# Kernel tuning notes

Hardware: AMD Instinct MI355X
Metric: run time of the kernel (lower is better)

Reference implementation:

```python
import jax, jax.numpy as jnp
import numpy as np

B, IN, OUT, BR = 64, 8192, 2048, 4
VTH = 0.5
_SQRT_2PI = float(np.sqrt(2.0 * np.pi))


def _gauss(x, mu, sigma):
    return jnp.exp(-((x - mu) ** 2) / (2.0 * sigma ** 2)) / _SQRT_2PI / sigma


@jax.custom_vjp
def act_fun(x):
    return (x > 0.0).astype(x.dtype)


def _act_fwd(x):
    return act_fun(x), x


def _act_bwd(x, g):
    lens, scale, hight, gamma = 0.5, 6.0, 0.15, 0.5
    temp = (_gauss(x, 0.0, lens) * (1.0 + hight)
            - _gauss(x, lens, scale * lens) * hight
            - _gauss(x, -lens, scale * lens) * hight)
    return (g * temp * gamma,)


act_fun.defvjp(_act_fwd, _act_bwd)


def setup_inputs() -> dict:
    key = jax.random.key(0)
    ks = jax.random.split(key, 8)
    fan_in = IN
    bound = 1.0 / np.sqrt(fan_in)
    return {
        "input_spike": jax.random.uniform(ks[0], (B, IN), dtype=jnp.float32),
        "mem": jax.random.uniform(ks[1], (B, OUT), dtype=jnp.float32),
        "spike": jax.random.uniform(ks[2], (B, OUT), dtype=jnp.float32),
        "d_input": jnp.zeros((B, OUT, BR), dtype=jnp.float32),
        "v_th": jnp.ones((B, OUT), dtype=jnp.float32) * VTH,
        "W": jax.random.uniform(ks[3], (OUT * BR, IN), minval=-bound, maxval=bound, dtype=jnp.float32),
        "b": jax.random.uniform(ks[4], (OUT * BR,), minval=-bound, maxval=bound, dtype=jnp.float32),
        "tau_m": jax.random.uniform(ks[5], (OUT,), minval=0.0, maxval=4.0, dtype=jnp.float32),
        "tau_n": jax.random.uniform(ks[6], (OUT, BR), minval=0.0, maxval=4.0, dtype=jnp.float32),
    }


def reference(input_spike, mem, spike, d_input, v_th, W, b, tau_m, tau_n):
    R_m = 1.0
    batch = input_spike.shape[0]
    out_dim, branch = tau_n.shape
    in_dim = W.shape[1]  # padded input size
    chunk = in_dim // branch
    # pad input to in_dim (pad == 0 for these dims, kept for generality)
    pad = in_dim - input_spike.shape[1]
    k = jnp.pad(input_spike.astype(jnp.float32), ((0, 0), (0, pad)))
    # block-masked linear: mask keeps, for neuron o / branch j, only column block j.
    # Equivalent to taking the diagonal blocks of W reshaped [out, branch, branch, chunk].
    W_diag = jnp.einsum("obbc->obc", W.reshape(out_dim, branch, branch, chunk))
    y = jnp.einsum("obc,nbc->nob", W_diag, k.reshape(batch, branch, chunk))
    y = y + b.reshape(out_dim, branch)  # [B, out, branch]
    # per-branch dendritic decay
    beta = jax.nn.sigmoid(tau_n)
    d_new = beta * d_input + (1.0 - beta) * y
    l_input = d_new.sum(axis=2)  # [B, out]
    # LIF with soft reset
    alpha = jax.nn.sigmoid(tau_m)
    mem_new = mem * alpha + (1.0 - alpha) * R_m * l_input - v_th * spike
    spike_new = act_fun(mem_new - v_th)
    return mem_new, spike_new
```

## Files before the change

### kernel.cpp

```cpp
#include <hip/hip_runtime.h>
#include <math.h>

#define BATCH   64
#define IN_DIM  8192
#define OUT_DIM 2048
#define BRANCH  4
#define CHUNK   2048
#define NSEG    2
#define KSEG    1024
#define KT      128
#define NT      8

typedef __attribute__((ext_vector_type(8))) short short8;
typedef __attribute__((ext_vector_type(4))) short short4v;
typedef __attribute__((ext_vector_type(4))) float f32x4;

__device__ __forceinline__ float sigmoidf_(float x) {
    return 1.0f / (1.0f + expf(-x));
}

__device__ __forceinline__ unsigned rne_bf16(float f) {
    unsigned u = __float_as_uint(f);
    return (u + 0x7fffu + ((u >> 16) & 1u)) >> 16;
}

#define LBAR()                                                   \
    do {                                                         \
        asm volatile("s_waitcnt lgkmcnt(0)" ::: "memory");       \
        __builtin_amdgcn_s_barrier();                            \
        asm volatile("" ::: "memory");                           \
    } while (0)

__global__ __launch_bounds__(256) void prep_x(const float* __restrict__ X,
                                              short8* __restrict__ Xfh,
                                              short8* __restrict__ Xfl) {
    const int gid = blockIdx.x * 256 + threadIdx.x;
    const int l  = gid & 63;
    const int kk = (gid >> 6) & 63;
    const int s  = (gid >> 12) & 3;
    const int j  = gid >> 14;
    const int n  = s * 16 + (l & 15);
    const int k0 = kk * 32 + ((l >> 4) << 3);
    const float* p = X + (size_t)n * IN_DIM + j * CHUNK + k0;
    const f32x4 a = *(const f32x4*)p;
    const f32x4 c = *(const f32x4*)(p + 4);
    float v[8] = {a[0], a[1], a[2], a[3], c[0], c[1], c[2], c[3]};
    short8 h, lo;
#pragma unroll
    for (int e = 0; e < 8; ++e) {
        unsigned hb = rne_bf16(v[e]);
        float fh = __uint_as_float(hb << 16);
        unsigned lb = rne_bf16(v[e] - fh);
        h[e]  = (short)hb;
        lo[e] = (short)lb;
    }
    Xfh[gid] = h;
    Xfl[gid] = lo;
}

__device__ __forceinline__ void stage_store(char* Wh, char* Wl, const f32x4* wr,
                                            int wbyte0, int swz, int kq) {
#pragma unroll
    for (int i = 0; i < 4; ++i) {
        unsigned hb[4], lb[4];
#pragma unroll
        for (int e = 0; e < 4; ++e) {
            const float f  = wr[i][e];
            const unsigned u  = __float_as_uint(f);
            const float fl = f - __uint_as_float(u & 0xffff0000u);
            hb[e] = u >> 16;
            lb[e] = __float_as_uint(fl) >> 16;
        }
        short4v vh = { (short)hb[0], (short)hb[1], (short)hb[2], (short)hb[3] };
        short4v vl = { (short)lb[0], (short)lb[1], (short)lb[2], (short)lb[3] };
        const int kb   = (kq << 5) + (i << 3);
        const int byte = wbyte0 + (kb ^ swz);
        *(short4v*)(Wh + byte) = vh;
        *(short4v*)(Wl + byte) = vl;
    }
}

__global__ __launch_bounds__(256) void dend_gemm(const short8* __restrict__ Xfh,
                                                 const short8* __restrict__ Xfl,
                                                 const float*  __restrict__ W,
                                                 float* __restrict__ Yp) {
    __shared__ __align__(16) char WhL[2][32 * 256];
    __shared__ __align__(16) char WlL[2][32 * 256];

    const int t    = threadIdx.x;
    const int bid  = blockIdx.x;
    const int j    = bid & 3;
    const int o0   = ((bid >> 2) & 63) << 5;
    const int ks   = bid >> 8;
    const int lane = t & 63;
    const int wv   = t >> 6;

    const int ri  = t >> 3;
    const int kq  = t & 7;
    const float* wsrc = W + (size_t)((o0 + ri) * 4 + j) * IN_DIM
                          + j * CHUNK + ks * KSEG + kq * 16;
    const int wbyte0 = ri << 8;
    const int swz    = (ri & 15) << 4;

    const short8* pAh = Xfh + (j * 4 + wv) * 4096 + ks * 2048 + lane;
    const short8* pAl = Xfl + (j * 4 + wv) * 4096 + ks * 2048 + lane;

    const int o_l   = lane & 15;
    const int bswz  = o_l << 4;
    const int kgrp  = (lane >> 4) << 4;
    const int b0row = o_l << 8;
    const int b1row = (o_l + 16) << 8;

    f32x4 acc0 = {0.f, 0.f, 0.f, 0.f};
    f32x4 acc1 = {0.f, 0.f, 0.f, 0.f};

    f32x4  wr[4];
    short8 Ah0[4], Al0[4], Ah1[4], Al1[4];

#pragma unroll
    for (int i = 0; i < 4; ++i)
        wr[i] = *(const f32x4*)(wsrc + i * 4);
    stage_store(WhL[0], WlL[0], wr, wbyte0, swz, kq);
#pragma unroll
    for (int i = 0; i < 4; ++i)
        wr[i] = *(const f32x4*)(wsrc + KT + i * 4);
#pragma unroll
    for (int i = 0; i < 4; ++i) { Ah0[i] = pAh[i * 64];       Al0[i] = pAl[i * 64]; }
#pragma unroll
    for (int i = 0; i < 4; ++i) { Ah1[i] = pAh[(4 + i) * 64]; Al1[i] = pAl[(4 + i) * 64]; }
    LBAR();

#define BODY(kt, AH, AL)                                                            \
  {                                                                                 \
    if ((kt) + 1 < NT)                                                              \
        stage_store(WhL[((kt) + 1) & 1], WlL[((kt) + 1) & 1], wr, wbyte0, swz, kq); \
    if ((kt) + 2 < NT) {                                                            \
        _Pragma("unroll")                                                           \
        for (int i = 0; i < 4; ++i)                                                 \
            wr[i] = *(const f32x4*)(wsrc + ((kt) + 2) * KT + i * 4);                \
    }                                                                               \
    _Pragma("unroll")                                                               \
    for (int st = 0; st < 4; ++st) {                                                \
        const int off = ((st << 6) + kgrp) ^ bswz;                                  \
        short8 bh0 = *(const short8*)(&WhL[(kt) & 1][b0row + off]);                 \
        short8 bl0 = *(const short8*)(&WlL[(kt) & 1][b0row + off]);                 \
        short8 bh1 = *(const short8*)(&WhL[(kt) & 1][b1row + off]);                 \
        short8 bl1 = *(const short8*)(&WlL[(kt) & 1][b1row + off]);                 \
        acc0 = __builtin_amdgcn_mfma_f32_16x16x32_bf16(AH[st], bh0, acc0, 0, 0, 0); \
        acc1 = __builtin_amdgcn_mfma_f32_16x16x32_bf16(AH[st], bh1, acc1, 0, 0, 0); \
        acc0 = __builtin_amdgcn_mfma_f32_16x16x32_bf16(AL[st], bh0, acc0, 0, 0, 0); \
        acc1 = __builtin_amdgcn_mfma_f32_16x16x32_bf16(AL[st], bh1, acc1, 0, 0, 0); \
        acc0 = __builtin_amdgcn_mfma_f32_16x16x32_bf16(AH[st], bl0, acc0, 0, 0, 0); \
        acc1 = __builtin_amdgcn_mfma_f32_16x16x32_bf16(AH[st], bl1, acc1, 0, 0, 0); \
    }                                                                               \
    if ((kt) + 2 < NT) {                                                            \
        _Pragma("unroll")                                                           \
        for (int i = 0; i < 4; ++i) {                                               \
            AH[i] = pAh[(((kt) + 2) * 4 + i) * 64];                                 \
            AL[i] = pAl[(((kt) + 2) * 4 + i) * 64];                                 \
        }                                                                           \
    }                                                                               \
    LBAR();                                                                         \
  }

#pragma unroll 1
    for (int kt = 0; kt < NT; kt += 2) {
        BODY(kt,     Ah0, Al0)
        BODY(kt + 1, Ah1, Al1)
    }
#undef BODY

    float (*Ys)[65] = (float (*)[65])(&WhL[0][0]);
    {
        const int rb = (wv << 4) + ((lane >> 4) << 2);
#pragma unroll
        for (int r = 0; r < 4; ++r) {
            Ys[o_l][rb + r]      = acc0[r];
            Ys[o_l + 16][rb + r] = acc1[r];
        }
    }
    __syncthreads();
#pragma unroll
    for (int p = 0; p < 8; ++p) {
        const int e  = t + (p << 8);
        const int oo = e & 31;
        const int n  = e >> 5;
        Yp[(size_t)(((ks * BATCH + n) << 2) + j) * OUT_DIM + o0 + oo] = Ys[oo][n];
    }
}

__global__ __launch_bounds__(256) void lif_pointwise(
    const float* __restrict__ Yp,
    const float* __restrict__ mem,
    const float* __restrict__ spike,
    const float* __restrict__ d_input,
    const float* __restrict__ v_th,
    const float* __restrict__ b,
    const float* __restrict__ tau_m,
    const float* __restrict__ tau_n,
    float* __restrict__ out)
{
    const int idx = blockIdx.x * 256 + threadIdx.x;
    const int o   = idx & (OUT_DIM - 1);
    const int n   = idx >> 11;

    const float4 tn = ((const float4*)tau_n)[o];
    const float4 bb = ((const float4*)b)[o];
    const float4 di = ((const float4*)d_input)[idx];

    float y0 = 0.f, y1 = 0.f, y2 = 0.f, y3 = 0.f;
#pragma unroll
    for (int s = 0; s < NSEG; ++s) {
        const size_t base = (size_t)((s * BATCH + n) << 2) * OUT_DIM + o;
        y0 += Yp[base];
        y1 += Yp[base + OUT_DIM];
        y2 += Yp[base + 2 * OUT_DIM];
        y3 += Yp[base + 3 * OUT_DIM];
    }

    float l = 0.0f;
    { const float bt = sigmoidf_(tn.x); l += bt * di.x + (1.0f - bt) * (y0 + bb.x); }
    { const float bt = sigmoidf_(tn.y); l += bt * di.y + (1.0f - bt) * (y1 + bb.y); }
    { const float bt = sigmoidf_(tn.z); l += bt * di.z + (1.0f - bt) * (y2 + bb.z); }
    { const float bt = sigmoidf_(tn.w); l += bt * di.w + (1.0f - bt) * (y3 + bb.w); }

    const float alpha = sigmoidf_(tau_m[o]);
    const float vt    = v_th[idx];
    const float m     = mem[idx] * alpha + (1.0f - alpha) * l - vt * spike[idx];

    out[idx] = m;
    out[BATCH * OUT_DIM + idx] = (m - vt) > 0.0f ? 1.0f : 0.0f;
}

extern "C" void kernel_launch(void* const* d_in, const int* in_sizes, int n_in,
                              void* d_out, int out_size, void* d_ws, size_t ws_size,
                              hipStream_t stream) {
    const float* X     = (const float*)d_in[0];
    const float* mem   = (const float*)d_in[1];
    const float* spike = (const float*)d_in[2];
    const float* dinp  = (const float*)d_in[3];
    const float* vth   = (const float*)d_in[4];
    const float* W     = (const float*)d_in[5];
    const float* b     = (const float*)d_in[6];
    const float* tm    = (const float*)d_in[7];
    const float* tn    = (const float*)d_in[8];
    float* out = (float*)d_out;

    short8* Xfh = (short8*)d_ws;
    short8* Xfl = (short8*)((char*)d_ws + (1u << 20));
    float*  Yp  = (float*)((char*)d_ws + (2u << 20));

    prep_x<<<256, 256, 0, stream>>>(X, Xfh, Xfl);
    dend_gemm<<<512, 256, 0, stream>>>(Xfh, Xfl, W, Yp);
    lif_pointwise<<<512, 256, 0, stream>>>(Yp, mem, spike, dinp, vth, b, tm, tn, out);
}
```

Baseline: 27.51 us.

## Double K tile to 256 and interleave A-fragment prefetch within each tile

Doubles the K-tile depth staged through LDS from 128 to 256, halving the number of barrier-separated iterations, and doubles the per-thread W register staging. The A-fragment loads are restructured so the second half of each tile is fetched while the first half computes, and the next tile's first half is fetched during the second half. This aims to cut barrier and sync overhead and improve overlap of global loads with MFMA. In exchange it doubles LDS use to 64KB and raises register pressure, which may reduce occupancy. The swizzle still only XORs the low 16-byte bits within the wider 512-byte rows.

```diff
diff --git a/kernel.cpp b/kernel.cpp
--- a/kernel.cpp
+++ b/kernel.cpp
@@ -8,8 +8,8 @@
 #define CHUNK   2048
 #define NSEG    2
 #define KSEG    1024
-#define KT      128
-#define NT      8
+#define KT      256
+#define NT      4
 
 typedef __attribute__((ext_vector_type(8))) short short8;
 typedef __attribute__((ext_vector_type(4))) short short4v;
@@ -61,7 +61,7 @@
 __device__ __forceinline__ void stage_store(char* Wh, char* Wl, const f32x4* wr,
                                             int wbyte0, int swz, int kq) {
 #pragma unroll
-    for (int i = 0; i < 4; ++i) {
+    for (int i = 0; i < 8; ++i) {
         unsigned hb[4], lb[4];
 #pragma unroll
         for (int e = 0; e < 4; ++e) {
@@ -73,7 +73,7 @@
         }
         short4v vh = { (short)hb[0], (short)hb[1], (short)hb[2], (short)hb[3] };
         short4v vl = { (short)lb[0], (short)lb[1], (short)lb[2], (short)lb[3] };
-        const int kb   = (kq << 5) + (i << 3);
+        const int kb   = (kq << 6) + (i << 3);
         const int byte = wbyte0 + (kb ^ swz);
         *(short4v*)(Wh + byte) = vh;
         *(short4v*)(Wl + byte) = vl;
@@ -84,8 +84,8 @@
                                                  const short8* __restrict__ Xfl,
                                                  const float*  __restrict__ W,
                                                  float* __restrict__ Yp) {
-    __shared__ __align__(16) char WhL[2][32 * 256];
-    __shared__ __align__(16) char WlL[2][32 * 256];
+    __shared__ __align__(16) char WhL[2][32 * 512];
+    __shared__ __align__(16) char WlL[2][32 * 512];
 
     const int t    = threadIdx.x;
     const int bid  = blockIdx.x;
@@ -98,8 +98,8 @@
     const int ri  = t >> 3;
     const int kq  = t & 7;
     const float* wsrc = W + (size_t)((o0 + ri) * 4 + j) * IN_DIM
-                          + j * CHUNK + ks * KSEG + kq * 16;
-    const int wbyte0 = ri << 8;
+                          + j * CHUNK + ks * KSEG + kq * 32;
+    const int wbyte0 = ri << 9;
     const int swz    = (ri & 15) << 4;
 
     const short8* pAh = Xfh + (j * 4 + wv) * 4096 + ks * 2048 + lane;
@@ -108,67 +108,71 @@
     const int o_l   = lane & 15;
     const int bswz  = o_l << 4;
     const int kgrp  = (lane >> 4) << 4;
-    const int b0row = o_l << 8;
-    const int b1row = (o_l + 16) << 8;
+    const int b0row = o_l << 9;
+    const int b1row = (o_l + 16) << 9;
 
     f32x4 acc0 = {0.f, 0.f, 0.f, 0.f};
     f32x4 acc1 = {0.f, 0.f, 0.f, 0.f};
 
-    f32x4  wr[4];
+    f32x4  wr[8];
     short8 Ah0[4], Al0[4], Ah1[4], Al1[4];
 
 #pragma unroll
-    for (int i = 0; i < 4; ++i)
+    for (int i = 0; i < 8; ++i)
         wr[i] = *(const f32x4*)(wsrc + i * 4);
     stage_store(WhL[0], WlL[0], wr, wbyte0, swz, kq);
 #pragma unroll
-    for (int i = 0; i < 4; ++i)
+    for (int i = 0; i < 8; ++i)
         wr[i] = *(const f32x4*)(wsrc + KT + i * 4);
 #pragma unroll
-    for (int i = 0; i < 4; ++i) { Ah0[i] = pAh[i * 64];       Al0[i] = pAl[i * 64]; }
-#pragma unroll
-    for (int i = 0; i < 4; ++i) { Ah1[i] = pAh[(4 + i) * 64]; Al1[i] = pAl[(4 + i) * 64]; }
+    for (int i = 0; i < 4; ++i) { Ah0[i] = pAh[i * 64]; Al0[i] = pAl[i * 64]; }
     LBAR();
 
-#define BODY(kt, AH, AL)                                                            \
-  {                                                                                 \
-    if ((kt) + 1 < NT)                                                              \
-        stage_store(WhL[((kt) + 1) & 1], WlL[((kt) + 1) & 1], wr, wbyte0, swz, kq); \
-    if ((kt) + 2 < NT) {                                                            \
-        _Pragma("unroll")                                                           \
-        for (int i = 0; i < 4; ++i)                                                 \
-            wr[i] = *(const f32x4*)(wsrc + ((kt) + 2) * KT + i * 4);                \
-    }                                                                               \
-    _Pragma("unroll")                                                               \
-    for (int st = 0; st < 4; ++st) {                                                \
-        const int off = ((st << 6) + kgrp) ^ bswz;                                  \
-        short8 bh0 = *(const short8*)(&WhL[(kt) & 1][b0row + off]);                 \
-        short8 bl0 = *(const short8*)(&WlL[(kt) & 1][b0row + off]);                 \
-        short8 bh1 = *(const short8*)(&WhL[(kt) & 1][b1row + off]);                 \
-        short8 bl1 = *(const short8*)(&WlL[(kt) & 1][b1row + off]);                 \
-        acc0 = __builtin_amdgcn_mfma_f32_16x16x32_bf16(AH[st], bh0, acc0, 0, 0, 0); \
-        acc1 = __builtin_amdgcn_mfma_f32_16x16x32_bf16(AH[st], bh1, acc1, 0, 0, 0); \
-        acc0 = __builtin_amdgcn_mfma_f32_16x16x32_bf16(AL[st], bh0, acc0, 0, 0, 0); \
-        acc1 = __builtin_amdgcn_mfma_f32_16x16x32_bf16(AL[st], bh1, acc1, 0, 0, 0); \
-        acc0 = __builtin_amdgcn_mfma_f32_16x16x32_bf16(AH[st], bl0, acc0, 0, 0, 0); \
-        acc1 = __builtin_amdgcn_mfma_f32_16x16x32_bf16(AH[st], bl1, acc1, 0, 0, 0); \
-    }                                                                               \
-    if ((kt) + 2 < NT) {                                                            \
-        _Pragma("unroll")                                                           \
-        for (int i = 0; i < 4; ++i) {                                               \
-            AH[i] = pAh[(((kt) + 2) * 4 + i) * 64];                                 \
-            AL[i] = pAl[(((kt) + 2) * 4 + i) * 64];                                 \
-        }                                                                           \
-    }                                                                               \
-    LBAR();                                                                         \
+#define STEP(AH, AL, sti, kt)                                                        \
+  {                                                                                  \
+    const int off = (((sti) << 6) + kgrp) ^ bswz;                                    \
+    short8 bh0 = *(const short8*)(&WhL[(kt) & 1][b0row + off]);                      \
+    short8 bl0 = *(const short8*)(&WlL[(kt) & 1][b0row + off]);                      \
+    short8 bh1 = *(const short8*)(&WhL[(kt) & 1][b1row + off]);                      \
+    short8 bl1 = *(const short8*)(&WlL[(kt) & 1][b1row + off]);                      \
+    acc0 = __builtin_amdgcn_mfma_f32_16x16x32_bf16(AH, bh0, acc0, 0, 0, 0);          \
+    acc1 = __builtin_amdgcn_mfma_f32_16x16x32_bf16(AH, bh1, acc1, 0, 0, 0);          \
+    acc0 = __builtin_amdgcn_mfma_f32_16x16x32_bf16(AL, bh0, acc0, 0, 0, 0);          \
+    acc1 = __builtin_amdgcn_mfma_f32_16x16x32_bf16(AL, bh1, acc1, 0, 0, 0);          \
+    acc0 = __builtin_amdgcn_mfma_f32_16x16x32_bf16(AH, bl0, acc0, 0, 0, 0);          \
+    acc1 = __builtin_amdgcn_mfma_f32_16x16x32_bf16(AH, bl1, acc1, 0, 0, 0);          \
   }
 
 #pragma unroll 1
-    for (int kt = 0; kt < NT; kt += 2) {
-        BODY(kt,     Ah0, Al0)
-        BODY(kt + 1, Ah1, Al1)
-    }
-#undef BODY
+    for (int kt = 0; kt < NT; ++kt) {
+        if (kt + 1 < NT)
+            stage_store(WhL[(kt + 1) & 1], WlL[(kt + 1) & 1], wr, wbyte0, swz, kq);
+        if (kt + 2 < NT) {
+#pragma unroll
+            for (int i = 0; i < 8; ++i)
+                wr[i] = *(const f32x4*)(wsrc + (kt + 2) * KT + i * 4);
+        }
+#pragma unroll
+        for (int i = 0; i < 4; ++i) {
+            Ah1[i] = pAh[(kt * 8 + 4 + i) * 64];
+            Al1[i] = pAl[(kt * 8 + 4 + i) * 64];
+        }
+#pragma unroll
+        for (int st = 0; st < 4; ++st)
+            STEP(Ah0[st], Al0[st], st, kt)
+        if (kt + 1 < NT) {
+#pragma unroll
+            for (int i = 0; i < 4; ++i) {
+                Ah0[i] = pAh[((kt + 1) * 8 + i) * 64];
+                Al0[i] = pAl[((kt + 1) * 8 + i) * 64];
+            }
+        }
+#pragma unroll
+        for (int st = 0; st < 4; ++st)
+            STEP(Ah1[st], Al1[st], st + 4, kt)
+        LBAR();
+    }
+#undef STEP
 
     float (*Ys)[65] = (float (*)[65])(&WhL[0][0]);
     {
```

New measurement: 32.67 us. +18.8%, slower.
